# Kernel tuning notes

Measured on AMD Instinct MI355X. Metric: run time of the kernel, lower is better.

## Reference

```python
import jax, jax.numpy as jnp
import numpy as np

N, D = 65536, 256

def setup_inputs() -> dict:
    key = jax.random.key(0)
    k1, k2, k3 = jax.random.split(key, 3)
    x = jax.random.normal(k1, (N, D), dtype=jnp.float32)
    x_fit = jax.random.normal(k2, (N, D), dtype=jnp.float32)
    # S_inv buffer: a symmetric PD-ish matrix (eye at init; use random SPD for generality)
    A = jax.random.normal(k3, (D, D), dtype=jnp.float32) / np.sqrt(D)
    S_inv = A @ A.T + jnp.eye(D, dtype=jnp.float32)
    return {"x": x, "x_fit": x_fit, "S_inv": S_inv}

def reference(x, x_fit, S_inv):
    # diag(delta @ S_inv @ delta.T) computed row-wise without the NxN intermediate
    delta = x - x_fit                     # [N, D]
    t = delta @ S_inv                     # [N, D]
    return jnp.sum(t * delta, axis=-1)    # [N]
```

## Files before the change

### kernel.cpp

```cpp
#include <hip/hip_runtime.h>
#include <hip/hip_bf16.h>
#include <stdint.h>


#define D 256
#define BLOCK_T 512
#define RPT 16
#define NT 8
#define LDS_STRIDE 272

typedef __attribute__((ext_vector_type(4))) float f32x4;
typedef __attribute__((ext_vector_type(8))) short bf16x8;
typedef __attribute__((ext_vector_type(4))) short bf16x4;

static __device__ __forceinline__ unsigned short f2bf(float f) {
    union { float f; uint32_t u; } v; v.f = f;
    uint32_t u = v.u;
    return (unsigned short)((u + 0x7FFFu + ((u >> 16) & 1u)) >> 16);
}
static __device__ __forceinline__ float bf2f(unsigned short s) {
    union { uint32_t u; float f; } v; v.u = ((uint32_t)s) << 16;
    return v.f;
}

static __device__ __forceinline__ f32x4 gload4f(const float* p) {
    f32x4 r;
    asm volatile("global_load_dwordx4 %0, %1, off" : "=v"(r) : "v"(p));
    return r;
}

__global__ void prep_S_kernel(const float* __restrict__ S, unsigned short* __restrict__ Sb) {
    int i = (blockIdx.x * 256 + threadIdx.x) * 4;
    f32x4 v = *(const f32x4*)(S + i);
    uint32_t lo = (uint32_t)f2bf(v[0]) | ((uint32_t)f2bf(v[1]) << 16);
    uint32_t hi = (uint32_t)f2bf(v[2]) | ((uint32_t)f2bf(v[3]) << 16);
    *(uint2*)(Sb + i) = make_uint2(lo, hi);
}

__global__ __launch_bounds__(BLOCK_T, 4) void mahal_kernel(
    const float* __restrict__ x, const float* __restrict__ xf,
    const unsigned short* __restrict__ Sb, float* __restrict__ out)
{
    __shared__ unsigned short ld[RPT * LDS_STRIDE];
    __shared__ float psum[8 * RPT];

    const int t    = threadIdx.x;
    const int w    = t >> 6;
    const int lane = t & 63;
    const int lo4  = lane & 15;
    const int kg   = lane >> 4;
    const int srow = t >> 5;
    const int scol = (t & 31) * 8;
    const int blockRow0 = blockIdx.x * (NT * RPT);

    f32x4 xs[2][2], fs[2][2];
    {
        const int g0 = (blockRow0 + srow) * D + scol;
        xs[0][0] = gload4f(x + g0);  xs[0][1] = gload4f(x + g0 + 4);
        fs[0][0] = gload4f(xf + g0); fs[0][1] = gload4f(xf + g0 + 4);
        const int g1 = (blockRow0 + RPT + srow) * D + scol;
        xs[1][0] = gload4f(x + g1);  xs[1][1] = gload4f(x + g1 + 4);
        fs[1][0] = gload4f(xf + g1); fs[1][1] = gload4f(xf + g1 + 4);
    }

    bf16x8 b0[8], b1[8];
    {
        const unsigned short* Sp = Sb + (w * 32 + lo4) * D + kg * 8;
        #pragma unroll
        for (int kb = 0; kb < 8; ++kb) {
            b0[kb] = *(const bf16x8*)(Sp + kb * 32);
            b1[kb] = *(const bf16x8*)(Sp + 16 * D + kb * 32);
        }
    }

    #pragma unroll
    for (int j = 0; j < NT; ++j) {
        const int bsel = j & 1;

        if (j < NT - 1) { asm volatile("s_waitcnt vmcnt(4)" ::: "memory"); }
        else            { asm volatile("s_waitcnt vmcnt(0)" ::: "memory"); }
        __builtin_amdgcn_sched_barrier(0);

        if (j > 0) {
            asm volatile("s_waitcnt lgkmcnt(0)" ::: "memory");
            __builtin_amdgcn_s_barrier();
            if (t < RPT) {
                float s = 0.f;
                #pragma unroll
                for (int ww = 0; ww < 8; ++ww) s += psum[ww * RPT + t];
                out[blockRow0 + (j - 1) * RPT + t] = s;
            }
        }

        {
            bf16x8 o;
            o[0] = (short)f2bf(xs[bsel][0][0] - fs[bsel][0][0]);
            o[1] = (short)f2bf(xs[bsel][0][1] - fs[bsel][0][1]);
            o[2] = (short)f2bf(xs[bsel][0][2] - fs[bsel][0][2]);
            o[3] = (short)f2bf(xs[bsel][0][3] - fs[bsel][0][3]);
            o[4] = (short)f2bf(xs[bsel][1][0] - fs[bsel][1][0]);
            o[5] = (short)f2bf(xs[bsel][1][1] - fs[bsel][1][1]);
            o[6] = (short)f2bf(xs[bsel][1][2] - fs[bsel][1][2]);
            o[7] = (short)f2bf(xs[bsel][1][3] - fs[bsel][1][3]);
            *(bf16x8*)(&ld[srow * LDS_STRIDE + scol]) = o;
        }

        if (j + 2 < NT) {
            const int g = (blockRow0 + (j + 2) * RPT + srow) * D + scol;
            xs[bsel][0] = gload4f(x + g);  xs[bsel][1] = gload4f(x + g + 4);
            fs[bsel][0] = gload4f(xf + g); fs[bsel][1] = gload4f(xf + g + 4);
        }

        asm volatile("s_waitcnt lgkmcnt(0)" ::: "memory");
        __builtin_amdgcn_s_barrier();
        __builtin_amdgcn_sched_barrier(0);

        {
            f32x4 acc0 = (f32x4){0.f, 0.f, 0.f, 0.f};
            f32x4 acc1 = (f32x4){0.f, 0.f, 0.f, 0.f};
            const unsigned short* A = &ld[lo4 * LDS_STRIDE + kg * 8];
            #pragma unroll
            for (int kb = 0; kb < 8; ++kb) {
                bf16x8 a = *(const bf16x8*)(A + kb * 32);
                acc0 = __builtin_amdgcn_mfma_f32_16x16x32_bf16(b0[kb], a, acc0, 0, 0, 0);
                acc1 = __builtin_amdgcn_mfma_f32_16x16x32_bf16(b1[kb], a, acc1, 0, 0, 0);
            }
            const unsigned short* dr = &ld[lo4 * LDS_STRIDE + w * 32 + kg * 4];
            bf16x4 d0 = *(const bf16x4*)(dr);
            bf16x4 d1 = *(const bf16x4*)(dr + 16);
            float pr = 0.f;
            #pragma unroll
            for (int r = 0; r < 4; ++r) {
                pr += acc0[r] * bf2f((unsigned short)d0[r]);
                pr += acc1[r] * bf2f((unsigned short)d1[r]);
            }
            pr += __shfl_xor(pr, 16, 64);
            pr += __shfl_xor(pr, 32, 64);
            if (lane < 16)
                psum[w * RPT + lane] = pr;
        }
    }

    asm volatile("s_waitcnt lgkmcnt(0)" ::: "memory");
    __builtin_amdgcn_s_barrier();
    if (t < RPT) {
        float s = 0.f;
        #pragma unroll
        for (int ww = 0; ww < 8; ++ww) s += psum[ww * RPT + t];
        out[blockRow0 + (NT - 1) * RPT + t] = s;
    }
}

extern "C" void kernel_launch(void* const* d_in, const int* in_sizes, int n_in,
                              void* d_out, int out_size, void* d_ws, size_t ws_size,
                              hipStream_t stream) {
    const float* x  = (const float*)d_in[0];
    const float* xf = (const float*)d_in[1];
    const float* S  = (const float*)d_in[2];
    float* out = (float*)d_out;
    unsigned short* Sb = (unsigned short*)d_ws;

    prep_S_kernel<<<(D * D) / (256 * 4), 256, 0, stream>>>(S, Sb);

    const int nRows = in_sizes[0] / D;
    const int nBlocks = nRows / (NT * RPT);
    mahal_kernel<<<nBlocks, BLOCK_T, 0, stream>>>(x, xf, Sb, out);
}
```

Baseline: 33.79 us.

## Stage inputs into LDS via direct global-to-LDS loads with 1024-thread blocks

Replaces register-staged global loads of x and x_fit with global_load_lds DMA into double-buffered fp32 LDS tiles. Block size doubles to 1024 threads, so each wave computes 16 output columns of the product with S instead of 32, halving the S registers held per wave. The final dot product now uses the fp32 delta read from LDS rather than the bf16-rounded copy, which improves accuracy. In exchange, LDS use is much higher and each stage now waits on vmcnt(0), which removes the previous two-deep register prefetch.

```diff
diff --git a/kernel.cpp b/kernel.cpp
--- a/kernel.cpp
+++ b/kernel.cpp
@@ -4,10 +4,11 @@
 
 
 #define D 256
-#define BLOCK_T 512
+#define BLOCK_T 1024
 #define RPT 16
 #define NT 8
-#define LDS_STRIDE 272
+#define BSTR 260
+#define TSTR 272
 
 typedef __attribute__((ext_vector_type(4))) float f32x4;
 typedef __attribute__((ext_vector_type(8))) short bf16x8;
@@ -18,15 +19,11 @@
     uint32_t u = v.u;
     return (unsigned short)((u + 0x7FFFu + ((u >> 16) & 1u)) >> 16);
 }
-static __device__ __forceinline__ float bf2f(unsigned short s) {
-    union { uint32_t u; float f; } v; v.u = ((uint32_t)s) << 16;
-    return v.f;
-}
 
-static __device__ __forceinline__ f32x4 gload4f(const float* p) {
-    f32x4 r;
-    asm volatile("global_load_dwordx4 %0, %1, off" : "=v"(r) : "v"(p));
-    return r;
+static __device__ __forceinline__ void gload_lds16(const float* g, void* l) {
+    __builtin_amdgcn_global_load_lds(
+        (const __attribute__((address_space(1))) void*)g,
+        (__attribute__((address_space(3))) void*)l, 16, 0, 0);
 }
 
 __global__ void prep_S_kernel(const float* __restrict__ S, unsigned short* __restrict__ Sb) {
@@ -37,78 +34,63 @@
     *(uint2*)(Sb + i) = make_uint2(lo, hi);
 }
 
-__global__ __launch_bounds__(BLOCK_T, 4) void mahal_kernel(
+__global__ __launch_bounds__(BLOCK_T, 8) void mahal_kernel(
     const float* __restrict__ x, const float* __restrict__ xf,
     const unsigned short* __restrict__ Sb, float* __restrict__ out)
 {
-    __shared__ unsigned short ld[RPT * LDS_STRIDE];
-    __shared__ float psum[8 * RPT];
+    __shared__ float xb[2][RPT][BSTR];
+    __shared__ float fb[2][RPT][BSTR];
+    __shared__ unsigned short ld[RPT * TSTR];
+    __shared__ float psum[16 * RPT];
 
     const int t    = threadIdx.x;
     const int w    = t >> 6;
     const int lane = t & 63;
     const int lo4  = lane & 15;
     const int kg   = lane >> 4;
-    const int srow = t >> 5;
-    const int scol = (t & 31) * 8;
     const int blockRow0 = blockIdx.x * (NT * RPT);
 
-    f32x4 xs[2][2], fs[2][2];
+    bf16x8 b[8];
     {
-        const int g0 = (blockRow0 + srow) * D + scol;
-        xs[0][0] = gload4f(x + g0);  xs[0][1] = gload4f(x + g0 + 4);
-        fs[0][0] = gload4f(xf + g0); fs[0][1] = gload4f(xf + g0 + 4);
-        const int g1 = (blockRow0 + RPT + srow) * D + scol;
-        xs[1][0] = gload4f(x + g1);  xs[1][1] = gload4f(x + g1 + 4);
-        fs[1][0] = gload4f(xf + g1); fs[1][1] = gload4f(xf + g1 + 4);
+        const unsigned short* Sp = Sb + (w * 16 + lo4) * D + kg * 8;
+        #pragma unroll
+        for (int kb = 0; kb < 8; ++kb) b[kb] = *(const bf16x8*)(Sp + kb * 32);
     }
 
-    bf16x8 b0[8], b1[8];
-    {
-        const unsigned short* Sp = Sb + (w * 32 + lo4) * D + kg * 8;
-        #pragma unroll
-        for (int kb = 0; kb < 8; ++kb) {
-            b0[kb] = *(const bf16x8*)(Sp + kb * 32);
-            b1[kb] = *(const bf16x8*)(Sp + 16 * D + kb * 32);
-        }
-    }
+    gload_lds16(x  + (blockRow0 + w) * D + lane * 4, &xb[0][w][0]);
+    gload_lds16(xf + (blockRow0 + w) * D + lane * 4, &fb[0][w][0]);
 
     #pragma unroll
     for (int j = 0; j < NT; ++j) {
-        const int bsel = j & 1;
+        const int cur = j & 1, nxt = cur ^ 1;
 
-        if (j < NT - 1) { asm volatile("s_waitcnt vmcnt(4)" ::: "memory"); }
-        else            { asm volatile("s_waitcnt vmcnt(0)" ::: "memory"); }
+        asm volatile("s_waitcnt vmcnt(0) lgkmcnt(0)" ::: "memory");
         __builtin_amdgcn_sched_barrier(0);
+        __builtin_amdgcn_s_barrier();
 
-        if (j > 0) {
-            asm volatile("s_waitcnt lgkmcnt(0)" ::: "memory");
-            __builtin_amdgcn_s_barrier();
-            if (t < RPT) {
-                float s = 0.f;
-                #pragma unroll
-                for (int ww = 0; ww < 8; ++ww) s += psum[ww * RPT + t];
-                out[blockRow0 + (j - 1) * RPT + t] = s;
-            }
+        if (j + 1 < NT) {
+            gload_lds16(x  + (blockRow0 + (j + 1) * RPT + w) * D + lane * 4, &xb[nxt][w][0]);
+            gload_lds16(xf + (blockRow0 + (j + 1) * RPT + w) * D + lane * 4, &fb[nxt][w][0]);
+        }
+
+        if (j > 0 && t < RPT) {
+            float s = 0.f;
+            #pragma unroll
+            for (int ww = 0; ww < 16; ++ww) s += psum[ww * RPT + t];
+            out[blockRow0 + (j - 1) * RPT + t] = s;
         }
 
         {
-            bf16x8 o;
-            o[0] = (short)f2bf(xs[bsel][0][0] - fs[bsel][0][0]);
-            o[1] = (short)f2bf(xs[bsel][0][1] - fs[bsel][0][1]);
-            o[2] = (short)f2bf(xs[bsel][0][2] - fs[bsel][0][2]);
-            o[3] = (short)f2bf(xs[bsel][0][3] - fs[bsel][0][3]);
-            o[4] = (short)f2bf(xs[bsel][1][0] - fs[bsel][1][0]);
-            o[5] = (short)f2bf(xs[bsel][1][1] - fs[bsel][1][1]);
-            o[6] = (short)f2bf(xs[bsel][1][2] - fs[bsel][1][2]);
-            o[7] = (short)f2bf(xs[bsel][1][3] - fs[bsel][1][3]);
-            *(bf16x8*)(&ld[srow * LDS_STRIDE + scol]) = o;
-        }
-
-        if (j + 2 < NT) {
-            const int g = (blockRow0 + (j + 2) * RPT + srow) * D + scol;
-            xs[bsel][0] = gload4f(x + g);  xs[bsel][1] = gload4f(x + g + 4);
-            fs[bsel][0] = gload4f(xf + g); fs[bsel][1] = gload4f(xf + g + 4);
+            const int cr = t >> 6;
+            const int cc = (t & 63) * 4;
+            f32x4 xv = *(const f32x4*)&xb[cur][cr][cc];
+            f32x4 fv = *(const f32x4*)&fb[cur][cr][cc];
+            bf16x4 o;
+            o[0] = (short)f2bf(xv[0] - fv[0]);
+            o[1] = (short)f2bf(xv[1] - fv[1]);
+            o[2] = (short)f2bf(xv[2] - fv[2]);
+            o[3] = (short)f2bf(xv[3] - fv[3]);
+            *(bf16x4*)&ld[cr * TSTR + cc] = o;
         }
 
         asm volatile("s_waitcnt lgkmcnt(0)" ::: "memory");
@@ -116,28 +98,20 @@
         __builtin_amdgcn_sched_barrier(0);
 
         {
-            f32x4 acc0 = (f32x4){0.f, 0.f, 0.f, 0.f};
-            f32x4 acc1 = (f32x4){0.f, 0.f, 0.f, 0.f};
-            const unsigned short* A = &ld[lo4 * LDS_STRIDE + kg * 8];
+            f32x4 acc = (f32x4){0.f, 0.f, 0.f, 0.f};
             #pragma unroll
             for (int kb = 0; kb < 8; ++kb) {
-                bf16x8 a = *(const bf16x8*)(A + kb * 32);
-                acc0 = __builtin_amdgcn_mfma_f32_16x16x32_bf16(b0[kb], a, acc0, 0, 0, 0);
-                acc1 = __builtin_amdgcn_mfma_f32_16x16x32_bf16(b1[kb], a, acc1, 0, 0, 0);
+                bf16x8 a = *(const bf16x8*)&ld[lo4 * TSTR + kb * 32 + kg * 8];
+                acc = __builtin_amdgcn_mfma_f32_16x16x32_bf16(b[kb], a, acc, 0, 0, 0);
             }
-            const unsigned short* dr = &ld[lo4 * LDS_STRIDE + w * 32 + kg * 4];
-            bf16x4 d0 = *(const bf16x4*)(dr);
-            bf16x4 d1 = *(const bf16x4*)(dr + 16);
+            f32x4 dx = *(const f32x4*)&xb[cur][lo4][w * 16 + kg * 4];
+            f32x4 df = *(const f32x4*)&fb[cur][lo4][w * 16 + kg * 4];
             float pr = 0.f;
             #pragma unroll
-            for (int r = 0; r < 4; ++r) {
-                pr += acc0[r] * bf2f((unsigned short)d0[r]);
-                pr += acc1[r] * bf2f((unsigned short)d1[r]);
-            }
+            for (int r = 0; r < 4; ++r) pr += acc[r] * (dx[r] - df[r]);
             pr += __shfl_xor(pr, 16, 64);
             pr += __shfl_xor(pr, 32, 64);
-            if (lane < 16)
-                psum[w * RPT + lane] = pr;
+            if (lane < 16) psum[w * RPT + lane] = pr;
         }
     }
 
@@ -146,7 +120,7 @@
     if (t < RPT) {
         float s = 0.f;
         #pragma unroll
-        for (int ww = 0; ww < 8; ++ww) s += psum[ww * RPT + t];
+        for (int ww = 0; ww < 16; ++ww) s += psum[ww * RPT + t];
         out[blockRow0 + (NT - 1) * RPT + t] = s;
     }
 }
```

Result: slower. 39.27 us, median of 2 (+16.2%).
